# Optimization experiments

Hardware: AMD Instinct MI355X
Metric: run time of the kernel (lower is better)

Reference implementation:

```python
import jax, jax.numpy as jnp
import numpy as np

N_NODES = 10000
N_EDGES = 64000
N_GRAPHS = 64
HID = 64


def _nnconv(h, src, dst, edge_attr, w1, b1, w2, b2, root, bias):
    # edge MLP: Linear(dim_edge,64) -> ReLU -> Linear(64, 64*64)
    we = (jax.nn.relu(edge_attr @ w1 + b1) @ w2 + b2).reshape(-1, HID, HID)  # [E,64,64]
    # per-edge matmul of gathered source features, then scatter-add to dst
    msg = jnp.einsum('ei,eio->eo', h[src], we)                               # [E,64]
    agg = jax.ops.segment_sum(msg, dst, num_segments=N_NODES)               # [N,64]
    return agg + h @ root + bias


def setup_inputs() -> dict:
    key = jax.random.key(0)
    ks = jax.random.split(key, 20)
    s = 0.05
    inp = {
        'x': jax.random.normal(ks[0], (N_NODES, 128), jnp.float32),
        'edge_index': jax.random.randint(ks[1], (2, N_EDGES), 0, N_NODES, dtype=jnp.int64),
        'edge_attr': jax.random.normal(ks[2], (N_EDGES, 32), jnp.float32),
        'batch': jnp.sort(jax.random.randint(ks[3], (N_NODES,), 0, N_GRAPHS, dtype=jnp.int64)),
        'nfc_w': jax.random.normal(ks[4], (128, HID), jnp.float32) * s,
        'nfc_b': jnp.zeros((HID,), jnp.float32),
        'efc1_w1': jax.random.normal(ks[5], (32, HID), jnp.float32) * s,
        'efc1_b1': jnp.zeros((HID,), jnp.float32),
        'efc1_w2': jax.random.normal(ks[6], (HID, HID * HID), jnp.float32) * s,
        'efc1_b2': jnp.zeros((HID * HID,), jnp.float32),
        'gc1_root': jax.random.normal(ks[7], (HID, HID), jnp.float32) * s,
        'gc1_bias': jnp.zeros((HID,), jnp.float32),
        'efc2_w1': jax.random.normal(ks[8], (32, HID), jnp.float32) * s,
        'efc2_b1': jnp.zeros((HID,), jnp.float32),
        'efc2_w2': jax.random.normal(ks[9], (HID, HID * HID), jnp.float32) * s,
        'efc2_b2': jnp.zeros((HID * HID,), jnp.float32),
        'gc2_root': jax.random.normal(ks[10], (HID, HID), jnp.float32) * s,
        'gc2_bias': jnp.zeros((HID,), jnp.float32),
        'fc1_w': jax.random.normal(ks[11], (HID, 32), jnp.float32) * s,
        'fc1_b': jnp.zeros((32,), jnp.float32),
        'fc2_w': jax.random.normal(ks[12], (32, 1), jnp.float32) * s,
        'fc2_b': jnp.zeros((1,), jnp.float32),
    }
    return inp


def reference(x, edge_index, edge_attr, batch,
              nfc_w, nfc_b,
              efc1_w1, efc1_b1, efc1_w2, efc1_b2, gc1_root, gc1_bias,
              efc2_w1, efc2_b1, efc2_w2, efc2_b2, gc2_root, gc2_bias,
              fc1_w, fc1_b, fc2_w, fc2_b):
    lrelu = lambda v: jax.nn.leaky_relu(v, 0.01)
    src, dst = edge_index[0], edge_index[1]
    hx = lrelu(x @ nfc_w + nfc_b)
    hx = lrelu(_nnconv(hx, src, dst, edge_attr, efc1_w1, efc1_b1, efc1_w2, efc1_b2, gc1_root, gc1_bias))
    hx = lrelu(_nnconv(hx, src, dst, edge_attr, efc2_w1, efc2_b1, efc2_w2, efc2_b2, gc2_root, gc2_bias))
    hg = jax.ops.segment_sum(hx, batch, num_segments=N_GRAPHS)  # global_add_pool -> [G,64]
    hg = lrelu(hg @ fc1_w + fc1_b)
    return hg @ fc2_w + fc2_b
```

## Files before the change

kernel.cpp:

```cpp
#include <hip/hip_runtime.h>
#include <hip/hip_bf16.h>

#define N_NODES  10000
#define N_EDGES  64000
#define N_GRAPHS 64
#define HID      64

typedef __attribute__((ext_vector_type(8))) short short8;
typedef __attribute__((ext_vector_type(4))) float f32x4;

__device__ __forceinline__ float lrelu(float v){ return v > 0.f ? v : 0.01f*v; }

__device__ __forceinline__ unsigned short f2bf(float f){
    union { float f; unsigned u; } v; v.f = f;
    unsigned r = v.u + 0x7fff + ((v.u >> 16) & 1);
    return (unsigned short)(r >> 16);
}
__device__ __forceinline__ float bf2f(unsigned short s){
    union { unsigned u; float f; } v; v.u = ((unsigned)s) << 16;
    return v.f;
}

#define PRE_NFC 2500
#define PRE_W2C 128
#define PRE_TR  4
#define PRE_CNT 250
__global__ void __launch_bounds__(256) pre_kernel(
        const float* __restrict__ x, const float* __restrict__ nfc_w, const float* __restrict__ nfc_b,
        float* __restrict__ hx1,
        const float* __restrict__ e1w2, unsigned short* __restrict__ w2t1,
        const float* __restrict__ e2w2, unsigned short* __restrict__ w2t2,
        const float* __restrict__ e1w1, unsigned short* __restrict__ w1t1,
        const float* __restrict__ e2w1, unsigned short* __restrict__ w1t2,
        const float* __restrict__ e1b2, unsigned short* __restrict__ b2t1,
        const float* __restrict__ e2b2, unsigned short* __restrict__ b2t2,
        const int* __restrict__ src, int* __restrict__ counts){
    __shared__ float tile[64][65];
    int b = blockIdx.x, tid = threadIdx.x;
    if (b < PRE_NFC){
        int m = tid & 63, n = b * 4 + (tid >> 6);
        float acc = nfc_b[m];
        const float* row = x + (size_t)n * 128;
        #pragma unroll 8
        for (int k = 0; k < 128; ++k) acc += row[k] * nfc_w[k * 64 + m];
        hx1[(size_t)n * 64 + m] = lrelu(acc);
    } else if (b < PRE_NFC + PRE_W2C){
        int bb = b - PRE_NFC;
        int k = bb & 63;
        const float* srcw = ((bb < 64) ? e1w2 : e2w2) + (size_t)k * 4096;
        unsigned short* dstw = (bb < 64) ? w2t1 : w2t2;
        for (int idx = tid; idx < 4096; idx += 256) tile[idx >> 6][idx & 63] = srcw[idx];
        __syncthreads();
        for (int idx = tid; idx < 4096; idx += 256){
            int o = idx >> 6, i = idx & 63;
            dstw[((size_t)(k * 64 + o) << 6) + i] = f2bf(tile[i][o]);
        }
    } else if (b < PRE_NFC + PRE_W2C + PRE_TR){
        int bb = b - PRE_NFC - PRE_W2C;
        if (bb < 2){
            const float* w1 = bb ? e2w1 : e1w1;
            unsigned short* w1t = bb ? w1t2 : w1t1;
            for (int idx = tid; idx < 2048; idx += 256){
                int o = idx >> 5, k = idx & 31;
                w1t[idx] = f2bf(w1[k * 64 + o]);
            }
        } else {
            const float* b2 = (bb == 3) ? e2b2 : e1b2;
            unsigned short* b2t = (bb == 3) ? b2t2 : b2t1;
            for (int idx = tid; idx < 4096; idx += 256){
                int o = idx >> 6, i = idx & 63;
                b2t[idx] = f2bf(b2[i * 64 + o]);
            }
        }
    } else {
        int e = (b - PRE_NFC - PRE_W2C - PRE_TR) * 256 + tid;
        if (e < N_EDGES) atomicAdd(&counts[src[e]], 1);
    }
}

__global__ void csr_scan_kernel(const int* __restrict__ counts, int* __restrict__ rowptr,
                                int* __restrict__ cursor){
    __shared__ int part[256];
    int tid = threadIdx.x;
    const int CH = (N_NODES + 255) / 256;
    int base = tid * CH, s = 0;
    for (int i = 0; i < CH; ++i){ int idx = base + i; if (idx < N_NODES){ cursor[idx] = 0; s += counts[idx]; } }
    part[tid] = s; __syncthreads();
    for (int off = 1; off < 256; off <<= 1){
        int v = (tid >= off) ? part[tid - off] : 0;
        __syncthreads();
        part[tid] += v;
        __syncthreads();
    }
    int run = part[tid] - s;
    for (int i = 0; i < CH; ++i){ int idx = base + i; if (idx < N_NODES){ rowptr[idx] = run; run += counts[idx]; } }
    if (tid == 255) rowptr[N_NODES] = run;
}

__global__ void csr_scatter_kernel(const int* __restrict__ src, const int* __restrict__ dst,
                                   const int* __restrict__ rowptr, int* __restrict__ cursor,
                                   int* __restrict__ eidx, int* __restrict__ dsts){
    int e = blockIdx.x * 256 + threadIdx.x;
    if (e >= N_EDGES) return;
    int s = src[e];
    int j = rowptr[s] + atomicAdd(&cursor[s], 1);
    eidx[j] = e; dsts[j] = dst[e];
}

#define NBT2 1000
#define NBH2 157
#define NBG  (157 * 8)
template<int L2FLAG>
__global__ void __launch_bounds__(256) layerA_kernel(
        const float* __restrict__ ea, const int* __restrict__ eidx,
        const unsigned short* __restrict__ w1t, const float* __restrict__ b1,
        unsigned short* __restrict__ tp,
        const float* __restrict__ hx, const unsigned short* __restrict__ b2t,
        float* __restrict__ hb2, float* __restrict__ agg,
        const unsigned short* __restrict__ w2t, unsigned short* __restrict__ G,
        float* __restrict__ hg){
    __shared__ unsigned short stg[64 * 256];
    int b = blockIdx.x, tid = threadIdx.x;
    int wid = tid >> 6, l = tid & 63;
    int m16 = l & 15, grp = l >> 4;

    if (b < NBT2){
        int j = b * 64 + wid * 16 + m16;
        const float* row = ea + (size_t)eidx[j] * 32 + grp * 8;
        float4 f0 = *(const float4*)(row);
        float4 f1 = *(const float4*)(row + 4);
        short8 ef;
        ef[0]=(short)f2bf(f0.x); ef[1]=(short)f2bf(f0.y); ef[2]=(short)f2bf(f0.z); ef[3]=(short)f2bf(f0.w);
        ef[4]=(short)f2bf(f1.x); ef[5]=(short)f2bf(f1.y); ef[6]=(short)f2bf(f1.z); ef[7]=(short)f2bf(f1.w);
        #pragma unroll
        for (int TB = 0; TB < 64; TB += 16){
            short8 wf = *(const short8*)(w1t + (TB + m16) * 32 + grp * 8);
            f32x4 acc = *(const f32x4*)(b1 + TB + grp * 4);
            acc = __builtin_amdgcn_mfma_f32_16x16x32_bf16(wf, ef, acc, 0, 0, 0);
            unsigned p0 = (unsigned)f2bf(fmaxf(acc[0], 0.f)) | ((unsigned)f2bf(fmaxf(acc[1], 0.f)) << 16);
            unsigned p1 = (unsigned)f2bf(fmaxf(acc[2], 0.f)) | ((unsigned)f2bf(fmaxf(acc[3], 0.f)) << 16);
            uint2 pk; pk.x = p0; pk.y = p1;
            *(uint2*)(tp + ((size_t)j << 6) + TB + grp * 4) = pk;
        }
    } else if (b < NBT2 + NBH2){
        int bb = b - NBT2;
        int node = bb * 64 + wid * 16 + m16;
        short8 h0 = {0,0,0,0,0,0,0,0}, h1 = {0,0,0,0,0,0,0,0};
        if (node < N_NODES){
            const float* hp = hx + ((size_t)node << 6) + grp * 8;
            float4 f0 = *(const float4*)(hp);
            float4 f1 = *(const float4*)(hp + 4);
            float4 f2 = *(const float4*)(hp + 32);
            float4 f3 = *(const float4*)(hp + 36);
            h0[0]=(short)f2bf(f0.x); h0[1]=(short)f2bf(f0.y); h0[2]=(short)f2bf(f0.z); h0[3]=(short)f2bf(f0.w);
            h0[4]=(short)f2bf(f1.x); h0[5]=(short)f2bf(f1.y); h0[6]=(short)f2bf(f1.z); h0[7]=(short)f2bf(f1.w);
            h1[0]=(short)f2bf(f2.x); h1[1]=(short)f2bf(f2.y); h1[2]=(short)f2bf(f2.z); h1[3]=(short)f2bf(f2.w);
            h1[4]=(short)f2bf(f3.x); h1[5]=(short)f2bf(f3.y); h1[6]=(short)f2bf(f3.z); h1[7]=(short)f2bf(f3.w);
        }
        #pragma unroll
        for (int TB = 0; TB < 64; TB += 16){
            short8 c0 = *(const short8*)(b2t + (TB + m16) * 64 + grp * 8);
            short8 c1 = *(const short8*)(b2t + (TB + m16) * 64 + 32 + grp * 8);
            f32x4 acc = {0.f, 0.f, 0.f, 0.f};
            acc = __builtin_amdgcn_mfma_f32_16x16x32_bf16(c0, h0, acc, 0, 0, 0);
            acc = __builtin_amdgcn_mfma_f32_16x16x32_bf16(c1, h1, acc, 0, 0, 0);
            if (node < N_NODES) *(f32x4*)(hb2 + ((size_t)node << 6) + TB + grp * 4) = acc;
        }
        f32x4 z = {0.f, 0.f, 0.f, 0.f};
        #pragma unroll
        for (int q = 0; q < 4; ++q){
            int chunk = q * 256 + tid;
            int n = bb * 64 + (chunk >> 4), c = (chunk & 15) * 4;
            if (n < N_NODES) *(f32x4*)(agg + ((size_t)n << 6) + c) = z;
        }
    } else if (b < NBT2 + NBH2 + NBG){
        int g = b - NBT2 - NBH2;
        int bx = g >> 3, by = g & 7;
        int n0 = bx * 64;
        int cb = by * 512;

        short8 bf0[4], bf1[4];
        #pragma unroll
        for (int ng = 0; ng < 4; ++ng){
            int node = n0 + ng * 16 + m16;
            short8 b0 = {0,0,0,0,0,0,0,0}, b1v = {0,0,0,0,0,0,0,0};
            if (node < N_NODES){
                const float* hp = hx + ((size_t)node << 6) + grp * 8;
                float4 f0 = *(const float4*)(hp);
                float4 f1 = *(const float4*)(hp + 4);
                float4 f2 = *(const float4*)(hp + 32);
                float4 f3 = *(const float4*)(hp + 36);
                b0[0]=(short)f2bf(f0.x); b0[1]=(short)f2bf(f0.y); b0[2]=(short)f2bf(f0.z); b0[3]=(short)f2bf(f0.w);
                b0[4]=(short)f2bf(f1.x); b0[5]=(short)f2bf(f1.y); b0[6]=(short)f2bf(f1.z); b0[7]=(short)f2bf(f1.w);
                b1v[0]=(short)f2bf(f2.x); b1v[1]=(short)f2bf(f2.y); b1v[2]=(short)f2bf(f2.z); b1v[3]=(short)f2bf(f2.w);
                b1v[4]=(short)f2bf(f3.x); b1v[5]=(short)f2bf(f3.y); b1v[6]=(short)f2bf(f3.z); b1v[7]=(short)f2bf(f3.w);
            }
            bf0[ng] = b0; bf1[ng] = b1v;
        }

        for (int h = 0; h < 2; ++h){
            #pragma unroll
            for (int tt = 0; tt < 4; ++tt){
                int t = h * 4 + tt;
                int TB = cb + t * 64 + wid * 16;
                const unsigned short* ap = w2t + ((size_t)(TB + m16) << 6) + grp * 8;
                short8 a0 = *(const short8*)ap;
                short8 a1 = *(const short8*)(ap + 32);
                int inrow = (tt * 128 + wid * 32 + grp * 8) ^ ((m16 & 7) << 4);
                #pragma unroll
                for (int ng = 0; ng < 4; ++ng){
                    f32x4 acc = {0.f, 0.f, 0.f, 0.f};
                    acc = __builtin_amdgcn_mfma_f32_16x16x32_bf16(a0, bf0[ng], acc, 0, 0, 0);
                    acc = __builtin_amdgcn_mfma_f32_16x16x32_bf16(a1, bf1[ng], acc, 0, 0, 0);
                    unsigned p0 = (unsigned)f2bf(acc[0]) | ((unsigned)f2bf(acc[1]) << 16);
                    unsigned p1 = (unsigned)f2bf(acc[2]) | ((unsigned)f2bf(acc[3]) << 16);
                    int row = ng * 16 + m16;
                    uint2 pk; pk.x = p0; pk.y = p1;
                    *(uint2*)((char*)stg + row * 512 + inrow) = pk;
                }
            }
            __syncthreads();
            #pragma unroll
            for (int s = 0; s < 8; ++s){
                int ci = s * 256 + tid;
                int row = ci >> 5;
                int node = n0 + row;
                uint4 v = *(uint4*)((char*)stg + row * 512 + (((ci & 31) * 16) ^ ((row & 7) << 4)));
                if (node < N_NODES)
                    *(uint4*)(G + ((size_t)node << 12) + cb + h * 256 + (ci & 31) * 8) = v;
            }
            __syncthreads();
        }
    } else if (L2FLAG){
        for (int i = tid; i < N_GRAPHS * 64; i += 256) hg[i] = 0.f;
    }
}

__global__ void __launch_bounds__(64) msg_csr_kernel(
        const unsigned short* __restrict__ tp, const unsigned short* __restrict__ G,
        const float* __restrict__ hb2, const int* __restrict__ rowptr,
        const int* __restrict__ dsts, float* __restrict__ agg){
    int s = blockIdx.x;
    int o = threadIdx.x;
    __shared__ unsigned short gl[4096];
    __shared__ unsigned short ts[64] __attribute__((aligned(16)));
    int r0 = rowptr[s], r1 = rowptr[s + 1];
    if (r0 == r1) return;
    const short8* gsrc = (const short8*)(G + ((size_t)s << 12));
    short8* gld = (short8*)gl;
    #pragma unroll
    for (int i = 0; i < 8; ++i) gld[i * 64 + o] = gsrc[i * 64 + o];
    float g[64];
    #pragma unroll
    for (int k = 0; k < 64; ++k) g[k] = bf2f(gl[k * 64 + o]);
    float hb = hb2[((size_t)s << 6) + o];
    for (int j = r0; j < r1; ++j){
        ts[o] = tp[((size_t)j << 6) + o];
        float acc = hb;
        #pragma unroll
        for (int k8 = 0; k8 < 8; ++k8){
            short8 tv = *(const short8*)&ts[k8 * 8];
            #pragma unroll
            for (int u = 0; u < 8; ++u) acc += bf2f((unsigned short)tv[u]) * g[k8 * 8 + u];
        }
        atomicAdd(&agg[((size_t)dsts[j] << 6) + o], acc);
    }
}

__global__ void combine_kernel(const float* __restrict__ agg, const float* __restrict__ hx,
                               const float* __restrict__ root, const float* __restrict__ bias,
                               float* __restrict__ out, int N){
    int m = threadIdx.x;
    int n = blockIdx.x * 4 + threadIdx.y;
    if (n >= N) return;
    float acc = agg[(size_t)n * 64 + m] + bias[m];
    const float* row = hx + (size_t)n * 64;
    #pragma unroll 8
    for (int k = 0; k < 64; ++k) acc += row[k] * root[k * 64 + m];
    out[(size_t)n * 64 + m] = lrelu(acc);
}

__global__ void combine2_kernel(const float* __restrict__ agg, const float* __restrict__ hx,
                                const float* __restrict__ root, const float* __restrict__ bias,
                                const int* __restrict__ batch, float* __restrict__ hg, int N){
    int m = threadIdx.x;
    int n = blockIdx.x * 4 + threadIdx.y;
    if (n >= N) return;
    float acc = agg[(size_t)n * 64 + m] + bias[m];
    const float* row = hx + (size_t)n * 64;
    #pragma unroll 8
    for (int k = 0; k < 64; ++k) acc += row[k] * root[k * 64 + m];
    atomicAdd(&hg[batch[n] * 64 + m], lrelu(acc));
}

__global__ void head_kernel(const float* __restrict__ hg, const float* __restrict__ fc1w,
                            const float* __restrict__ fc1b, const float* __restrict__ fc2w,
                            const float* __restrict__ fc2b, float* __restrict__ out){
    int g = threadIdx.x;
    const float* row = hg + g * 64;
    float h1[32];
    #pragma unroll
    for (int j = 0; j < 32; ++j){
        float a = fc1b[j];
        #pragma unroll 8
        for (int i = 0; i < 64; ++i) a += row[i] * fc1w[i * 32 + j];
        h1[j] = lrelu(a);
    }
    float o = fc2b[0];
    #pragma unroll
    for (int j = 0; j < 32; ++j) o += h1[j] * fc2w[j];
    out[g] = o;
}

extern "C" void kernel_launch(void* const* d_in, const int* in_sizes, int n_in,
                              void* d_out, int out_size, void* d_ws, size_t ws_size,
                              hipStream_t stream){
    const float* x      = (const float*)d_in[0];
    const int*   ei     = (const int*)  d_in[1];
    const float* ea     = (const float*)d_in[2];
    const int*   batch  = (const int*)  d_in[3];
    const float* nfc_w  = (const float*)d_in[4];
    const float* nfc_b  = (const float*)d_in[5];
    const float* e1w1   = (const float*)d_in[6];
    const float* e1b1   = (const float*)d_in[7];
    const float* e1w2   = (const float*)d_in[8];
    const float* e1b2   = (const float*)d_in[9];
    const float* g1root = (const float*)d_in[10];
    const float* g1bias = (const float*)d_in[11];
    const float* e2w1   = (const float*)d_in[12];
    const float* e2b1   = (const float*)d_in[13];
    const float* e2w2   = (const float*)d_in[14];
    const float* e2b2   = (const float*)d_in[15];
    const float* g2root = (const float*)d_in[16];
    const float* g2bias = (const float*)d_in[17];
    const float* fc1w   = (const float*)d_in[18];
    const float* fc1b   = (const float*)d_in[19];
    const float* fc2w   = (const float*)d_in[20];
    const float* fc2b   = (const float*)d_in[21];
    float* out = (float*)d_out;

    const int* src = ei;
    const int* dst = ei + N_EDGES;

    char* ws = (char*)d_ws;
    float* hx1 = (float*)ws;               ws += (size_t)N_NODES * 64 * 4;
    float* hx2 = (float*)ws;               ws += (size_t)N_NODES * 64 * 4;
    unsigned short* tp = (unsigned short*)ws; ws += (size_t)N_EDGES * 64 * 2;
    float* hb2 = (float*)ws;               ws += (size_t)N_NODES * 64 * 4;
    float* agg = (float*)ws;               ws += (size_t)N_NODES * 64 * 4;
    float* hg  = (float*)ws;               ws += (size_t)N_GRAPHS * 64 * 4;
    unsigned short* w2t1 = (unsigned short*)ws; ws += (size_t)64 * 64 * 64 * 2;
    unsigned short* w2t2 = (unsigned short*)ws; ws += (size_t)64 * 64 * 64 * 2;
    unsigned short* w1t1 = (unsigned short*)ws; ws += (size_t)2048 * 2;
    unsigned short* w1t2 = (unsigned short*)ws; ws += (size_t)2048 * 2;
    unsigned short* b2t1 = (unsigned short*)ws; ws += (size_t)4096 * 2;
    unsigned short* b2t2 = (unsigned short*)ws; ws += (size_t)4096 * 2;
    int* counts = (int*)ws;                ws += (size_t)10240 * 4;
    int* cursor = (int*)ws;                ws += (size_t)10240 * 4;
    int* rowptr = (int*)ws;                ws += (size_t)10240 * 4;
    int* eidx   = (int*)ws;                ws += (size_t)N_EDGES * 4;
    int* dsts   = (int*)ws;                ws += (size_t)N_EDGES * 4;
    unsigned short* G = (unsigned short*)ws;

    dim3 blk(64, 4);

    hipMemsetAsync(counts, 0, (size_t)N_NODES * 4, stream);
    pre_kernel<<<PRE_NFC + PRE_W2C + PRE_TR + PRE_CNT, 256, 0, stream>>>(
        x, nfc_w, nfc_b, hx1, e1w2, w2t1, e2w2, w2t2,
        e1w1, w1t1, e2w1, w1t2, e1b2, b2t1, e2b2, b2t2, src, counts);
    csr_scan_kernel<<<1, 256, 0, stream>>>(counts, rowptr, cursor);
    csr_scatter_kernel<<<N_EDGES / 256, 256, 0, stream>>>(src, dst, rowptr, cursor, eidx, dsts);

    layerA_kernel<0><<<NBT2 + NBH2 + NBG, 256, 0, stream>>>(
        ea, eidx, w1t1, e1b1, tp, hx1, b2t1, hb2, agg, w2t1, G, nullptr);
    msg_csr_kernel<<<N_NODES, 64, 0, stream>>>(tp, G, hb2, rowptr, dsts, agg);
    combine_kernel<<<N_NODES / 4, blk, 0, stream>>>(agg, hx1, g1root, g1bias, hx2, N_NODES);

    layerA_kernel<1><<<NBT2 + NBH2 + NBG + 1, 256, 0, stream>>>(
        ea, eidx, w1t2, e2b1, tp, hx2, b2t2, hb2, agg, w2t2, G, hg);
    msg_csr_kernel<<<N_NODES, 64, 0, stream>>>(tp, G, hb2, rowptr, dsts, agg);
    combine2_kernel<<<N_NODES / 4, blk, 0, stream>>>(agg, hx2, g2root, g2bias, batch, hg, N_NODES);

    head_kernel<<<1, 64, 0, stream>>>(hg, fc1w, fc1b, fc2w, fc2b, out);
}
```

Before: 254.2 us.

## Fuse per-node G computation into CSR message kernel, drop G round-trip

Per-node G matrices (h @ W2, 64x4096 per node) were previously written to global memory in bf16 by layerA and read back by msg_csr. They are now computed in shared memory inside a fused kernel that handles 16 nodes per block, with each block covering one half of the output columns. This removes roughly 80 MB of global writes and reads per layer. The node feature Linear is also moved onto bf16 MFMA, and the counts memset plus small weight transposes are folded into a separate init kernel. As a trade-off, each edge's atomics to agg are split across two blocks, and the fused kernel uses 64KB of LDS, which limits occupancy.

After: 300.2 us. +18.1%, slower.

```diff
diff --git a/kernel.cpp b/kernel.cpp
--- a/kernel.cpp
+++ b/kernel.cpp
@@ -20,30 +20,84 @@
     union { unsigned u; float f; } v; v.u = ((unsigned)s) << 16;
     return v.f;
 }
-
-#define PRE_NFC 2500
-#define PRE_W2C 128
-#define PRE_TR  4
-#define PRE_CNT 250
-__global__ void __launch_bounds__(256) pre_kernel(
-        const float* __restrict__ x, const float* __restrict__ nfc_w, const float* __restrict__ nfc_b,
-        float* __restrict__ hx1,
-        const float* __restrict__ e1w2, unsigned short* __restrict__ w2t1,
-        const float* __restrict__ e2w2, unsigned short* __restrict__ w2t2,
+__device__ __forceinline__ short8 pack_bf8(float4 a, float4 b){
+    short8 r;
+    r[0]=(short)f2bf(a.x); r[1]=(short)f2bf(a.y); r[2]=(short)f2bf(a.z); r[3]=(short)f2bf(a.w);
+    r[4]=(short)f2bf(b.x); r[5]=(short)f2bf(b.y); r[6]=(short)f2bf(b.z); r[7]=(short)f2bf(b.w);
+    return r;
+}
+
+__global__ void __launch_bounds__(256) init_kernel(
+        int* __restrict__ counts,
+        const float* __restrict__ nfc_w, unsigned short* __restrict__ nfc_wt,
         const float* __restrict__ e1w1, unsigned short* __restrict__ w1t1,
         const float* __restrict__ e2w1, unsigned short* __restrict__ w1t2,
         const float* __restrict__ e1b2, unsigned short* __restrict__ b2t1,
-        const float* __restrict__ e2b2, unsigned short* __restrict__ b2t2,
+        const float* __restrict__ e2b2, unsigned short* __restrict__ b2t2){
+    int b = blockIdx.x, tid = threadIdx.x;
+    if (b < 40){
+        int i = b * 256 + tid;
+        if (i < N_NODES) counts[i] = 0;
+    } else if (b == 40){
+        for (int idx = tid; idx < 8192; idx += 256){
+            int o = idx >> 7, i = idx & 127;
+            nfc_wt[idx] = f2bf(nfc_w[i * 64 + o]);
+        }
+    } else if (b <= 42){
+        const float* w1 = (b == 42) ? e2w1 : e1w1;
+        unsigned short* w1t = (b == 42) ? w1t2 : w1t1;
+        for (int idx = tid; idx < 2048; idx += 256){
+            int o = idx >> 5, k = idx & 31;
+            w1t[idx] = f2bf(w1[k * 64 + o]);
+        }
+    } else {
+        const float* b2 = (b == 44) ? e2b2 : e1b2;
+        unsigned short* b2t = (b == 44) ? b2t2 : b2t1;
+        for (int idx = tid; idx < 4096; idx += 256){
+            int o = idx >> 6, i = idx & 63;
+            b2t[idx] = f2bf(b2[i * 64 + o]);
+        }
+    }
+}
+
+#define PRE_NFC 157
+#define PRE_W2C 128
+#define PRE_CNT 250
+__global__ void __launch_bounds__(256) pre_kernel(
+        const float* __restrict__ x, const unsigned short* __restrict__ nfc_wt,
+        const float* __restrict__ nfc_b, float* __restrict__ hx1,
+        const float* __restrict__ e1w2, unsigned short* __restrict__ w2t1,
+        const float* __restrict__ e2w2, unsigned short* __restrict__ w2t2,
         const int* __restrict__ src, int* __restrict__ counts){
     __shared__ float tile[64][65];
     int b = blockIdx.x, tid = threadIdx.x;
+    int wid = tid >> 6, l = tid & 63;
+    int m16 = l & 15, grp = l >> 4;
     if (b < PRE_NFC){
-        int m = tid & 63, n = b * 4 + (tid >> 6);
-        float acc = nfc_b[m];
-        const float* row = x + (size_t)n * 128;
-        #pragma unroll 8
-        for (int k = 0; k < 128; ++k) acc += row[k] * nfc_w[k * 64 + m];
-        hx1[(size_t)n * 64 + m] = lrelu(acc);
+        int node = b * 64 + wid * 16 + m16;
+        bool ok = node < N_NODES;
+        short8 xb[4];
+        #pragma unroll
+        for (int kq = 0; kq < 4; ++kq){
+            if (ok){
+                const float* xp = x + (size_t)node * 128 + kq * 32 + grp * 8;
+                xb[kq] = pack_bf8(*(const float4*)xp, *(const float4*)(xp + 4));
+            } else {
+                short8 z = {0,0,0,0,0,0,0,0}; xb[kq] = z;
+            }
+        }
+        #pragma unroll
+        for (int TB = 0; TB < 64; TB += 16){
+            f32x4 acc = *(const f32x4*)(nfc_b + TB + grp * 4);
+            #pragma unroll
+            for (int kq = 0; kq < 4; ++kq){
+                short8 af = *(const short8*)(nfc_wt + (TB + m16) * 128 + kq * 32 + grp * 8);
+                acc = __builtin_amdgcn_mfma_f32_16x16x32_bf16(af, xb[kq], acc, 0, 0, 0);
+            }
+            f32x4 r;
+            r[0] = lrelu(acc[0]); r[1] = lrelu(acc[1]); r[2] = lrelu(acc[2]); r[3] = lrelu(acc[3]);
+            if (ok) *(f32x4*)(hx1 + ((size_t)node << 6) + TB + grp * 4) = r;
+        }
     } else if (b < PRE_NFC + PRE_W2C){
         int bb = b - PRE_NFC;
         int k = bb & 63;
@@ -55,25 +109,8 @@
             int o = idx >> 6, i = idx & 63;
             dstw[((size_t)(k * 64 + o) << 6) + i] = f2bf(tile[i][o]);
         }
-    } else if (b < PRE_NFC + PRE_W2C + PRE_TR){
-        int bb = b - PRE_NFC - PRE_W2C;
-        if (bb < 2){
-            const float* w1 = bb ? e2w1 : e1w1;
-            unsigned short* w1t = bb ? w1t2 : w1t1;
-            for (int idx = tid; idx < 2048; idx += 256){
-                int o = idx >> 5, k = idx & 31;
-                w1t[idx] = f2bf(w1[k * 64 + o]);
-            }
-        } else {
-            const float* b2 = (bb == 3) ? e2b2 : e1b2;
-            unsigned short* b2t = (bb == 3) ? b2t2 : b2t1;
-            for (int idx = tid; idx < 4096; idx += 256){
-                int o = idx >> 6, i = idx & 63;
-                b2t[idx] = f2bf(b2[i * 64 + o]);
-            }
-        }
     } else {
-        int e = (b - PRE_NFC - PRE_W2C - PRE_TR) * 256 + tid;
+        int e = (b - PRE_NFC - PRE_W2C) * 256 + tid;
         if (e < N_EDGES) atomicAdd(&counts[src[e]], 1);
     }
 }
@@ -109,17 +146,13 @@
 
 #define NBT2 1000
 #define NBH2 157
-#define NBG  (157 * 8)
 template<int L2FLAG>
-__global__ void __launch_bounds__(256) layerA_kernel(
+__global__ void __launch_bounds__(256) layerB_kernel(
         const float* __restrict__ ea, const int* __restrict__ eidx,
         const unsigned short* __restrict__ w1t, const float* __restrict__ b1,
         unsigned short* __restrict__ tp,
         const float* __restrict__ hx, const unsigned short* __restrict__ b2t,
-        float* __restrict__ hb2, float* __restrict__ agg,
-        const unsigned short* __restrict__ w2t, unsigned short* __restrict__ G,
-        float* __restrict__ hg){
-    __shared__ unsigned short stg[64 * 256];
+        float* __restrict__ hb2, float* __restrict__ agg, float* __restrict__ hg){
     int b = blockIdx.x, tid = threadIdx.x;
     int wid = tid >> 6, l = tid & 63;
     int m16 = l & 15, grp = l >> 4;
@@ -127,11 +160,7 @@
     if (b < NBT2){
         int j = b * 64 + wid * 16 + m16;
         const float* row = ea + (size_t)eidx[j] * 32 + grp * 8;
-        float4 f0 = *(const float4*)(row);
-        float4 f1 = *(const float4*)(row + 4);
-        short8 ef;
-        ef[0]=(short)f2bf(f0.x); ef[1]=(short)f2bf(f0.y); ef[2]=(short)f2bf(f0.z); ef[3]=(short)f2bf(f0.w);
-        ef[4]=(short)f2bf(f1.x); ef[5]=(short)f2bf(f1.y); ef[6]=(short)f2bf(f1.z); ef[7]=(short)f2bf(f1.w);
+        short8 ef = pack_bf8(*(const float4*)row, *(const float4*)(row + 4));
         #pragma unroll
         for (int TB = 0; TB < 64; TB += 16){
             short8 wf = *(const short8*)(w1t + (TB + m16) * 32 + grp * 8);
@@ -148,14 +177,8 @@
         short8 h0 = {0,0,0,0,0,0,0,0}, h1 = {0,0,0,0,0,0,0,0};
         if (node < N_NODES){
             const float* hp = hx + ((size_t)node << 6) + grp * 8;
-            float4 f0 = *(const float4*)(hp);
-            float4 f1 = *(const float4*)(hp + 4);
-            float4 f2 = *(const float4*)(hp + 32);
-            float4 f3 = *(const float4*)(hp + 36);
-            h0[0]=(short)f2bf(f0.x); h0[1]=(short)f2bf(f0.y); h0[2]=(short)f2bf(f0.z); h0[3]=(short)f2bf(f0.w);
-            h0[4]=(short)f2bf(f1.x); h0[5]=(short)f2bf(f1.y); h0[6]=(short)f2bf(f1.z); h0[7]=(short)f2bf(f1.w);
-            h1[0]=(short)f2bf(f2.x); h1[1]=(short)f2bf(f2.y); h1[2]=(short)f2bf(f2.z); h1[3]=(short)f2bf(f2.w);
-            h1[4]=(short)f2bf(f3.x); h1[5]=(short)f2bf(f3.y); h1[6]=(short)f2bf(f3.z); h1[7]=(short)f2bf(f3.w);
+            h0 = pack_bf8(*(const float4*)hp, *(const float4*)(hp + 4));
+            h1 = pack_bf8(*(const float4*)(hp + 32), *(const float4*)(hp + 36));
         }
         #pragma unroll
         for (int TB = 0; TB < 64; TB += 16){
@@ -173,97 +196,73 @@
             int n = bb * 64 + (chunk >> 4), c = (chunk & 15) * 4;
             if (n < N_NODES) *(f32x4*)(agg + ((size_t)n << 6) + c) = z;
         }
-    } else if (b < NBT2 + NBH2 + NBG){
-        int g = b - NBT2 - NBH2;
-        int bx = g >> 3, by = g & 7;
-        int n0 = bx * 64;
-        int cb = by * 512;
-
-        short8 bf0[4], bf1[4];
-        #pragma unroll
-        for (int ng = 0; ng < 4; ++ng){
-            int node = n0 + ng * 16 + m16;
-            short8 b0 = {0,0,0,0,0,0,0,0}, b1v = {0,0,0,0,0,0,0,0};
-            if (node < N_NODES){
-                const float* hp = hx + ((size_t)node << 6) + grp * 8;
-                float4 f0 = *(const float4*)(hp);
-                float4 f1 = *(const float4*)(hp + 4);
-                float4 f2 = *(const float4*)(hp + 32);
-                float4 f3 = *(const float4*)(hp + 36);
-                b0[0]=(short)f2bf(f0.x); b0[1]=(short)f2bf(f0.y); b0[2]=(short)f2bf(f0.z); b0[3]=(short)f2bf(f0.w);
-                b0[4]=(short)f2bf(f1.x); b0[5]=(short)f2bf(f1.y); b0[6]=(short)f2bf(f1.z); b0[7]=(short)f2bf(f1.w);
-                b1v[0]=(short)f2bf(f2.x); b1v[1]=(short)f2bf(f2.y); b1v[2]=(short)f2bf(f2.z); b1v[3]=(short)f2bf(f2.w);
-                b1v[4]=(short)f2bf(f3.x); b1v[5]=(short)f2bf(f3.y); b1v[6]=(short)f2bf(f3.z); b1v[7]=(short)f2bf(f3.w);
-            }
-            bf0[ng] = b0; bf1[ng] = b1v;
-        }
-
-        for (int h = 0; h < 2; ++h){
-            #pragma unroll
-            for (int tt = 0; tt < 4; ++tt){
-                int t = h * 4 + tt;
-                int TB = cb + t * 64 + wid * 16;
-                const unsigned short* ap = w2t + ((size_t)(TB + m16) << 6) + grp * 8;
-                short8 a0 = *(const short8*)ap;
-                short8 a1 = *(const short8*)(ap + 32);
-                int inrow = (tt * 128 + wid * 32 + grp * 8) ^ ((m16 & 7) << 4);
-                #pragma unroll
-                for (int ng = 0; ng < 4; ++ng){
-                    f32x4 acc = {0.f, 0.f, 0.f, 0.f};
-                    acc = __builtin_amdgcn_mfma_f32_16x16x32_bf16(a0, bf0[ng], acc, 0, 0, 0);
-                    acc = __builtin_amdgcn_mfma_f32_16x16x32_bf16(a1, bf1[ng], acc, 0, 0, 0);
-                    unsigned p0 = (unsigned)f2bf(acc[0]) | ((unsigned)f2bf(acc[1]) << 16);
-                    unsigned p1 = (unsigned)f2bf(acc[2]) | ((unsigned)f2bf(acc[3]) << 16);
-                    int row = ng * 16 + m16;
-                    uint2 pk; pk.x = p0; pk.y = p1;
-                    *(uint2*)((char*)stg + row * 512 + inrow) = pk;
-                }
-            }
-            __syncthreads();
-            #pragma unroll
-            for (int s = 0; s < 8; ++s){
-                int ci = s * 256 + tid;
-                int row = ci >> 5;
-                int node = n0 + row;
-                uint4 v = *(uint4*)((char*)stg + row * 512 + (((ci & 31) * 16) ^ ((row & 7) << 4)));
-                if (node < N_NODES)
-                    *(uint4*)(G + ((size_t)node << 12) + cb + h * 256 + (ci & 31) * 8) = v;
-            }
-            __syncthreads();
-        }
     } else if (L2FLAG){
         for (int i = tid; i < N_GRAPHS * 64; i += 256) hg[i] = 0.f;
     }
 }
 
-__global__ void __launch_bounds__(64) msg_csr_kernel(
-        const unsigned short* __restrict__ tp, const unsigned short* __restrict__ G,
-        const float* __restrict__ hb2, const int* __restrict__ rowptr,
-        const int* __restrict__ dsts, float* __restrict__ agg){
-    int s = blockIdx.x;
-    int o = threadIdx.x;
-    __shared__ unsigned short gl[4096];
-    __shared__ unsigned short ts[64] __attribute__((aligned(16)));
-    int r0 = rowptr[s], r1 = rowptr[s + 1];
-    if (r0 == r1) return;
-    const short8* gsrc = (const short8*)(G + ((size_t)s << 12));
-    short8* gld = (short8*)gl;
+__global__ void __launch_bounds__(512) fused_kernel(
+        const float* __restrict__ hx, const unsigned short* __restrict__ w2t,
+        const unsigned short* __restrict__ tp, const float* __restrict__ hb2,
+        const int* __restrict__ rowptr, const int* __restrict__ dsts,
+        float* __restrict__ agg){
+    __shared__ unsigned short stg[16 * 2048];
+    int tid = threadIdx.x;
+    int wid = tid >> 6, l = tid & 63;
+    int m16 = l & 15, grp = l >> 4;
+    int bx = blockIdx.x >> 1, half = blockIdx.x & 1;
+    int n0 = bx * 16;
+    int cb = half * 2048;
+
+    const float* hp = hx + ((size_t)(n0 + m16) << 6) + grp * 8;
+    short8 b0 = pack_bf8(*(const float4*)hp, *(const float4*)(hp + 4));
+    short8 b1 = pack_bf8(*(const float4*)(hp + 32), *(const float4*)(hp + 36));
+
+    #pragma unroll 4
+    for (int tt = 0; tt < 16; ++tt){
+        int TB = cb + (wid * 16 + tt) * 16;
+        const unsigned short* ap = w2t + ((size_t)(TB + m16) << 6) + grp * 8;
+        short8 a0 = *(const short8*)ap;
+        short8 a1 = *(const short8*)(ap + 32);
+        f32x4 acc = {0.f, 0.f, 0.f, 0.f};
+        acc = __builtin_amdgcn_mfma_f32_16x16x32_bf16(a0, b0, acc, 0, 0, 0);
+        acc = __builtin_amdgcn_mfma_f32_16x16x32_bf16(a1, b1, acc, 0, 0, 0);
+        unsigned p0 = (unsigned)f2bf(acc[0]) | ((unsigned)f2bf(acc[1]) << 16);
+        unsigned p1 = (unsigned)f2bf(acc[2]) | ((unsigned)f2bf(acc[3]) << 16);
+        int row = m16;
+        int colLocal = (TB - cb) + grp * 4;
+        int off = (row * 4096 + colLocal * 2) ^ ((row & 7) << 4);
+        uint2 pk; pk.x = p0; pk.y = p1;
+        *(uint2*)((char*)stg + off) = pk;
+    }
+    __syncthreads();
+
     #pragma unroll
-    for (int i = 0; i < 8; ++i) gld[i * 64 + o] = gsrc[i * 64 + o];
-    float g[64];
-    #pragma unroll
-    for (int k = 0; k < 64; ++k) g[k] = bf2f(gl[k * 64 + o]);
-    float hb = hb2[((size_t)s << 6) + o];
-    for (int j = r0; j < r1; ++j){
-        ts[o] = tp[((size_t)j << 6) + o];
-        float acc = hb;
-        #pragma unroll
-        for (int k8 = 0; k8 < 8; ++k8){
-            short8 tv = *(const short8*)&ts[k8 * 8];
+    for (int q = 0; q < 2; ++q){
+        int ln = wid * 2 + q;
+        int s = n0 + ln;
+        int r0 = rowptr[s], r1 = rowptr[s + 1];
+        if (r0 == r1) continue;
+        float gk[32];
+        #pragma unroll
+        for (int kk = 0; kk < 32; ++kk){
+            int off = (ln * 4096 + (kk * 64 + l) * 2) ^ ((ln & 7) << 4);
+            gk[kk] = bf2f(*(const unsigned short*)((const char*)stg + off));
+        }
+        float hb = half ? 0.f : hb2[((size_t)s << 6) + l];
+        for (int j = r0; j < r1; ++j){
+            const short8* tpe = (const short8*)(tp + ((size_t)j << 6) + half * 32);
+            short8 t0 = tpe[0], t1 = tpe[1], t2 = tpe[2], t3 = tpe[3];
+            float acc = hb;
             #pragma unroll
-            for (int u = 0; u < 8; ++u) acc += bf2f((unsigned short)tv[u]) * g[k8 * 8 + u];
-        }
-        atomicAdd(&agg[((size_t)dsts[j] << 6) + o], acc);
+            for (int u = 0; u < 8; ++u){
+                acc += bf2f((unsigned short)t0[u]) * gk[u];
+                acc += bf2f((unsigned short)t1[u]) * gk[8 + u];
+                acc += bf2f((unsigned short)t2[u]) * gk[16 + u];
+                acc += bf2f((unsigned short)t3[u]) * gk[24 + u];
+            }
+            atomicAdd(&agg[((size_t)dsts[j] << 6) + l], acc);
+        }
     }
 }
 
@@ -351,6 +350,7 @@
     float* hg  = (float*)ws;               ws += (size_t)N_GRAPHS * 64 * 4;
     unsigned short* w2t1 = (unsigned short*)ws; ws += (size_t)64 * 64 * 64 * 2;
     unsigned short* w2t2 = (unsigned short*)ws; ws += (size_t)64 * 64 * 64 * 2;
+    unsigned short* nfc_wt = (unsigned short*)ws; ws += (size_t)8192 * 2;
     unsigned short* w1t1 = (unsigned short*)ws; ws += (size_t)2048 * 2;
     unsigned short* w1t2 = (unsigned short*)ws; ws += (size_t)2048 * 2;
     unsigned short* b2t1 = (unsigned short*)ws; ws += (size_t)4096 * 2;
@@ -360,25 +360,24 @@
     int* rowptr = (int*)ws;                ws += (size_t)10240 * 4;
     int* eidx   = (int*)ws;                ws += (size_t)N_EDGES * 4;
     int* dsts   = (int*)ws;                ws += (size_t)N_EDGES * 4;
-    unsigned short* G = (unsigned short*)ws;
 
     dim3 blk(64, 4);
 
-    hipMemsetAsync(counts, 0, (size_t)N_NODES * 4, stream);
-    pre_kernel<<<PRE_NFC + PRE_W2C + PRE_TR + PRE_CNT, 256, 0, stream>>>(
-        x, nfc_w, nfc_b, hx1, e1w2, w2t1, e2w2, w2t2,
-        e1w1, w1t1, e2w1, w1t2, e1b2, b2t1, e2b2, b2t2, src, counts);
+    init_kernel<<<45, 256, 0, stream>>>(counts, nfc_w, nfc_wt,
+                                        e1w1, w1t1, e2w1, w1t2, e1b2, b2t1, e2b2, b2t2);
+    pre_kernel<<<PRE_NFC + PRE_W2C + PRE_CNT, 256, 0, stream>>>(
+        x, nfc_wt, nfc_b, hx1, e1w2, w2t1, e2w2, w2t2, src, counts);
     csr_scan_kernel<<<1, 256, 0, stream>>>(counts, rowptr, cursor);
     csr_scatter_kernel<<<N_EDGES / 256, 256, 0, stream>>>(src, dst, rowptr, cursor, eidx, dsts);
 
-    layerA_kernel<0><<<NBT2 + NBH2 + NBG, 256, 0, stream>>>(
-        ea, eidx, w1t1, e1b1, tp, hx1, b2t1, hb2, agg, w2t1, G, nullptr);
-    msg_csr_kernel<<<N_NODES, 64, 0, stream>>>(tp, G, hb2, rowptr, dsts, agg);
+    layerB_kernel<0><<<NBT2 + NBH2, 256, 0, stream>>>(
+        ea, eidx, w1t1, e1b1, tp, hx1, b2t1, hb2, agg, nullptr);
+    fused_kernel<<<1250, 512, 0, stream>>>(hx1, w2t1, tp, hb2, rowptr, dsts, agg);
     combine_kernel<<<N_NODES / 4, blk, 0, stream>>>(agg, hx1, g1root, g1bias, hx2, N_NODES);
 
-    layerA_kernel<1><<<NBT2 + NBH2 + NBG + 1, 256, 0, stream>>>(
-        ea, eidx, w1t2, e2b1, tp, hx2, b2t2, hb2, agg, w2t2, G, hg);
-    msg_csr_kernel<<<N_NODES, 64, 0, stream>>>(tp, G, hb2, rowptr, dsts, agg);
+    layerB_kernel<1><<<NBT2 + NBH2 + 1, 256, 0, stream>>>(
+        ea, eidx, w1t2, e2b1, tp, hx2, b2t2, hb2, agg, hg);
+    fused_kernel<<<1250, 512, 0, stream>>>(hx2, w2t2, tp, hb2, rowptr, dsts, agg);
     combine2_kernel<<<N_NODES / 4, blk, 0, stream>>>(agg, hx2, g2root, g2bias, batch, hg, N_NODES);
 
     head_kernel<<<1, 64, 0, stream>>>(hg, fc1w, fc1b, fc2w, fc2b, out);
```
